# Performance work log

Measured on AMD Instinct MI355X. Metric: run time of the kernel, lower is better.

The kernel has to match this reference:

```python
import jax, jax.numpy as jnp
import numpy as np

N_NODES = 100000
N_EDGES = 1600000
D_IN = 128
D_H = 128
D_OUT = 64


def _glorot(key, shape):
    fan_in, fan_out = shape[0], shape[1]
    lim = np.sqrt(6.0 / (fan_in + fan_out)).astype(np.float32)
    return jax.random.uniform(key, shape, jnp.float32, -lim, lim)


def setup_inputs() -> dict:
    key = jax.random.key(0)
    ks = jax.random.split(key, 12)
    x = jax.random.normal(ks[0], (N_NODES, D_IN), jnp.float32)
    edge_index = jax.random.randint(ks[1], (2, N_EDGES), 0, N_NODES, jnp.int64)
    return {
        'x': x,
        'edge_index': edge_index,
        'Wl0': _glorot(ks[2], (D_IN, D_H)),  'bl0': jnp.zeros((D_H,), jnp.float32), 'Wr0': _glorot(ks[3], (D_IN, D_H)),
        'Wl1': _glorot(ks[4], (D_H, D_H)),   'bl1': jnp.zeros((D_H,), jnp.float32), 'Wr1': _glorot(ks[5], (D_H, D_H)),
        'Wl2': _glorot(ks[6], (D_H, D_H)),   'bl2': jnp.zeros((D_H,), jnp.float32), 'Wr2': _glorot(ks[7], (D_H, D_H)),
        'W':   _glorot(ks[8], (D_H, D_OUT)), 'b':   jnp.zeros((D_OUT,), jnp.float32),
    }


def _sage_conv(x, src, dst, inv_deg, Wl, bl, Wr):
    # mean aggregation of neighbor features at dst, then lin_l(agg) + lin_r(x)
    agg = jax.ops.segment_sum(x[src], dst, num_segments=N_NODES)  # [N, d]
    mean = agg * inv_deg  # [N, d]
    return mean @ Wl + bl + x @ Wr


def reference(x, edge_index, Wl0, bl0, Wr0, Wl1, bl1, Wr1, Wl2, bl2, Wr2, W, b):
    src, dst = edge_index[0], edge_index[1]
    deg = jax.ops.segment_sum(jnp.ones((N_EDGES,), jnp.float32), dst, num_segments=N_NODES)
    inv_deg = (1.0 / jnp.maximum(deg, 1.0))[:, None]  # [N, 1]
    h = jax.nn.relu(_sage_conv(x, src, dst, inv_deg, Wl0, bl0, Wr0))
    h = jax.nn.relu(_sage_conv(h, src, dst, inv_deg, Wl1, bl1, Wr1))
    h = jax.nn.relu(_sage_conv(h, src, dst, inv_deg, Wl2, bl2, Wr2))
    return h @ W + b
```

## Files before the change

### kernel.cpp

```cpp
#include <hip/hip_runtime.h>
#include <cstddef>

#define N_NODES 100000
#define N_EDGES 1600000
#define D 128
#define NB 782
#define CAP 3072
#define NBLK 1000
#define CHUNK 1600
#define WTOT (6 * 16384 + 8192)

typedef unsigned int u32;
typedef unsigned long long u64;
typedef float f32x4 __attribute__((ext_vector_type(4)));
typedef _Float16 f16x8 __attribute__((ext_vector_type(8)));

__device__ inline f16x8 mk16(u64 a, u64 b) {
  union { u64 q[2]; f16x8 v; } u;
  u.q[0] = a; u.q[1] = b;
  return u.v;
}

__device__ inline void acc8(float* a, uint2 d, float c) {
  a[0] += (float)(d.x & 0xFFu) * c;
  a[1] += (float)((d.x >> 8) & 0xFFu) * c;
  a[2] += (float)((d.x >> 16) & 0xFFu) * c;
  a[3] += (float)(d.x >> 24) * c;
  a[4] += (float)(d.y & 0xFFu) * c;
  a[5] += (float)((d.y >> 8) & 0xFFu) * c;
  a[6] += (float)((d.y >> 16) & 0xFFu) * c;
  a[7] += (float)(d.y >> 24) * c;
}


__global__ __launch_bounds__(256) void k_prep(
    const float* __restrict__ x, unsigned short* __restrict__ x16,
    unsigned char* __restrict__ x8, float* __restrict__ sx,
    const float* __restrict__ w0, const float* __restrict__ w1, const float* __restrict__ w2,
    const float* __restrict__ w3, const float* __restrict__ w4, const float* __restrict__ w5,
    const float* __restrict__ w6, unsigned short* __restrict__ wt16,
    int* __restrict__ bucket_cur) {
  int bid = blockIdx.x;
  int tid = threadIdx.x;
  if (bid < 6250) {
    int row = bid * 16 + (tid >> 4);
    int sub = tid & 15;
    const float* xr = x + (size_t)row * D + sub * 8;
    float4 v0 = *(const float4*)xr;
    float4 v1 = *(const float4*)(xr + 4);
    float vs[8] = {v0.x, v0.y, v0.z, v0.w, v1.x, v1.y, v1.z, v1.w};
    f16x8 h;
#pragma unroll
    for (int j = 0; j < 8; j++) h[j] = (_Float16)vs[j];
    *(uint4*)(x16 + (size_t)row * D + sub * 8) = __builtin_bit_cast(uint4, h);
    float m = 0.f;
#pragma unroll
    for (int j = 0; j < 8; j++) m = fmaxf(m, fabsf(vs[j]));
#pragma unroll
    for (int off = 1; off < 16; off <<= 1) m = fmaxf(m, __shfl_xor(m, off));
    m = fmaxf(m, 1e-8f);
    float inv = 127.0f / m;
    u64 pk = 0;
#pragma unroll
    for (int j = 0; j < 8; j++) {
      int qi = (int)rintf(vs[j] * inv) + 128;
      pk |= (u64)(u32)(qi & 255) << (8 * j);
    }
    *(u64*)(x8 + (size_t)row * D + sub * 8) = pk;
    if (sub == 0) sx[row] = m / 127.0f;
    return;
  }
  int i = (bid - 6250) * 256 + tid;
  if (i < NB) bucket_cur[i] = i * CAP;
  if (i >= WTOT) return;
  float v;
  if (i < 6 * 16384) {
    int m = i >> 14;
    int j = i & 16383;
    int c = j >> 7, k = j & 127;
    const float* w = (m == 0) ? w0 : (m == 1) ? w1 : (m == 2) ? w2
                   : (m == 3) ? w3 : (m == 4) ? w4 : w5;
    v = w[k * 128 + c];
  } else {
    int j = i - 6 * 16384;
    int c = j >> 7, k = j & 127;
    v = w6[k * 64 + c];
  }
  _Float16 h = (_Float16)v;
  wt16[i] = __builtin_bit_cast(unsigned short, h);
}


__global__ __launch_bounds__(256) void k_scatter(const int* __restrict__ src,
                                                 const int* __restrict__ dst,
                                                 int* __restrict__ bucket_cur,
                                                 u32* __restrict__ binned) {
  __shared__ int cnt[NB];
  __shared__ int base[NB];
  for (int i = threadIdx.x; i < NB; i += 256) cnt[i] = 0;
  __syncthreads();
  int e0 = blockIdx.x * CHUNK;
  for (int e = e0 + threadIdx.x; e < e0 + CHUNK; e += 256)
    atomicAdd(&cnt[dst[e] >> 7], 1);
  __syncthreads();
  for (int i = threadIdx.x; i < NB; i += 256) {
    int c = cnt[i];
    base[i] = c ? atomicAdd(&bucket_cur[i], c) : 0;
  }
  __syncthreads();
  for (int i = threadIdx.x; i < NB; i += 256) cnt[i] = 0;
  __syncthreads();
  for (int e = e0 + threadIdx.x; e < e0 + CHUNK; e += 256) {
    int d = dst[e];
    int b = d >> 7;
    int pos = base[b] + atomicAdd(&cnt[b], 1);
    binned[pos] = ((u32)(d & 127) << 17) | (u32)src[e];
  }
}

__global__ __launch_bounds__(256) void k_build(const u32* __restrict__ binned,
                                               const int* __restrict__ bucket_cur,
                                               int* __restrict__ row_start,
                                               int* __restrict__ row_end,
                                               float* __restrict__ inv_deg,
                                               int* __restrict__ csr_src) {
  __shared__ int deg[128], sc[128], cur[128];
  int b = blockIdx.x;
  int tid = threadIdx.x;
  int nbase = b << 7;
  int e0 = b * CAP, e1 = bucket_cur[b];
  if (tid < 128) deg[tid] = 0;
  __syncthreads();
  for (int e = e0 + tid; e < e1; e += 256)
    atomicAdd(&deg[binned[e] >> 17], 1);
  __syncthreads();
  int dv = (tid < 128) ? deg[tid] : 0;
  if (tid < 128) sc[tid] = dv;
  __syncthreads();
  for (int off = 1; off < 128; off <<= 1) {
    int t = (tid >= off && tid < 128) ? sc[tid - off] : 0;
    __syncthreads();
    if (tid < 128) sc[tid] += t;
    __syncthreads();
  }
  if (tid < 128) {
    int excl = sc[tid] - dv;
    cur[tid] = excl;
    int node = nbase + tid;
    if (node < N_NODES) {
      row_start[node] = e0 + excl;
      row_end[node] = e0 + excl + dv;
      inv_deg[node] = 1.0f / fmaxf((float)dv, 1.0f);
    }
  }
  __syncthreads();
  for (int e = e0 + tid; e < e1; e += 256) {
    u32 w = binned[e];
    int dl = w >> 17;
    int pos = e0 + atomicAdd(&cur[dl], 1);
    csr_src[pos] = (int)(w & 0x1FFFFu);
  }
}


template <bool BIASED>
__global__ __launch_bounds__(256) void k_agg(const unsigned char* __restrict__ q8,
                                             const float* __restrict__ qs,
                                             const int* __restrict__ row_start,
                                             const int* __restrict__ row_end,
                                             const float* __restrict__ inv_deg,
                                             const int* __restrict__ csr_src,
                                             unsigned short* __restrict__ out16) {
  int node = blockIdx.x * 16 + (threadIdx.x >> 4);
  if (node >= N_NODES) return;
  int sub = threadIdx.x & 15;
  int p0 = row_start[node], p1 = row_end[node];
  float a[8];
#pragma unroll
  for (int j = 0; j < 8; j++) a[j] = 0.f;
  float ssum = 0.f;
  int p = p0;
  for (; p + 8 <= p1; p += 8) {
    int s0 = csr_src[p], s1 = csr_src[p + 1], s2 = csr_src[p + 2], s3 = csr_src[p + 3];
    int s4 = csr_src[p + 4], s5 = csr_src[p + 5], s6 = csr_src[p + 6], s7 = csr_src[p + 7];
    uint2 d0 = *(const uint2*)(q8 + (size_t)s0 * D + sub * 8);
    uint2 d1 = *(const uint2*)(q8 + (size_t)s1 * D + sub * 8);
    uint2 d2 = *(const uint2*)(q8 + (size_t)s2 * D + sub * 8);
    uint2 d3 = *(const uint2*)(q8 + (size_t)s3 * D + sub * 8);
    uint2 d4 = *(const uint2*)(q8 + (size_t)s4 * D + sub * 8);
    uint2 d5 = *(const uint2*)(q8 + (size_t)s5 * D + sub * 8);
    uint2 d6 = *(const uint2*)(q8 + (size_t)s6 * D + sub * 8);
    uint2 d7 = *(const uint2*)(q8 + (size_t)s7 * D + sub * 8);
    float c0 = qs[s0], c1 = qs[s1], c2 = qs[s2], c3 = qs[s3];
    float c4 = qs[s4], c5 = qs[s5], c6 = qs[s6], c7 = qs[s7];
    acc8(a, d0, c0); acc8(a, d1, c1); acc8(a, d2, c2); acc8(a, d3, c3);
    acc8(a, d4, c4); acc8(a, d5, c5); acc8(a, d6, c6); acc8(a, d7, c7);
    if (BIASED) ssum += ((c0 + c1) + (c2 + c3)) + ((c4 + c5) + (c6 + c7));
  }
  for (; p + 2 <= p1; p += 2) {
    int s0 = csr_src[p], s1 = csr_src[p + 1];
    uint2 d0 = *(const uint2*)(q8 + (size_t)s0 * D + sub * 8);
    uint2 d1 = *(const uint2*)(q8 + (size_t)s1 * D + sub * 8);
    float c0 = qs[s0], c1 = qs[s1];
    acc8(a, d0, c0); acc8(a, d1, c1);
    if (BIASED) ssum += c0 + c1;
  }
  if (p < p1) {
    int s0 = csr_src[p];
    uint2 d0 = *(const uint2*)(q8 + (size_t)s0 * D + sub * 8);
    float c0 = qs[s0];
    acc8(a, d0, c0);
    if (BIASED) ssum += c0;
  }
  float scl = inv_deg[node];
  f16x8 o;
#pragma unroll
  for (int j = 0; j < 8; j++) {
    float v = a[j];
    if (BIASED) v -= 128.0f * ssum;
    o[j] = (_Float16)(v * scl);
  }
  *(uint4*)(out16 + (size_t)node * D + sub * 8) = __builtin_bit_cast(uint4, o);
}


__global__ __launch_bounds__(256) void k_gemm(
    const unsigned short* __restrict__ in0, const unsigned short* __restrict__ in1,
    const unsigned short* __restrict__ wt, const float* __restrict__ bias,
    unsigned short* __restrict__ outp,
    unsigned char* __restrict__ h8out, float* __restrict__ shout) {
  __shared__ u64 sI[128][9];
  __shared__ u64 sW[128][9];
  __shared__ u32 rmaxb[128];
  __shared__ unsigned char h8t[128 * 144];

  const int tid = threadIdx.x;
  const int row0 = blockIdx.x * 128;
  const int lane = tid & 63;
  const int w = tid >> 6;
  const int wr = w >> 1, wc = w & 1;
  const int lrow = lane & 15, kb = lane >> 4;
  const int sr = tid >> 2, sq = tid & 3;

  f32x4 acc[4][4];
#pragma unroll
  for (int i = 0; i < 4; i++)
#pragma unroll
    for (int j = 0; j < 4; j++) acc[i][j] = (f32x4){0.f, 0.f, 0.f, 0.f};

  u64 rA[2][2], rW[2][2];

  auto loadA = [&](int ch) {
    const unsigned short* inP = (ch >= 4) ? in1 : in0;
    const int kc = (ch & 3) * 32;
#pragma unroll
    for (int it = 0; it < 2; ++it) {
      int g = row0 + sr + it * 64;
      u64 a = 0, b = 0;
      if (g < N_NODES) {
        const u64* pp = (const u64*)(inP + (size_t)g * D + kc + sq * 8);
        a = pp[0]; b = pp[1];
      }
      rA[it][0] = a; rA[it][1] = b;
    }
  };
  auto loadW = [&](int ch) {
    const int s = ch >> 2;
    const int kc = (ch & 3) * 32;
    const unsigned short* wP = wt + (size_t)s * 16384;
#pragma unroll
    for (int it = 0; it < 2; ++it) {
      int c = sr + it * 64;
      const u64* pp = (const u64*)(wP + (size_t)c * D + kc + sq * 8);
      rW[it][0] = pp[0]; rW[it][1] = pp[1];
    }
  };

  loadA(0); loadW(0);
#pragma unroll
  for (int ch = 0; ch < 8; ++ch) {
    __syncthreads();
#pragma unroll
    for (int it = 0; it < 2; ++it) {
      int r = sr + it * 64;
      sI[r][sq * 2] = rA[it][0]; sI[r][sq * 2 + 1] = rA[it][1];
      sW[r][sq * 2] = rW[it][0]; sW[r][sq * 2 + 1] = rW[it][1];
    }
    __syncthreads();
    if (ch < 7) { loadA(ch + 1); loadW(ch + 1); }

    f16x8 fA[4], fB[4];
#pragma unroll
    for (int rt = 0; rt < 4; ++rt) {
      int rr = wr * 64 + rt * 16 + lrow;
      fA[rt] = mk16(sI[rr][kb * 2], sI[rr][kb * 2 + 1]);
    }
#pragma unroll
    for (int ct = 0; ct < 4; ++ct) {
      int cc = wc * 64 + ct * 16 + lrow;
      fB[ct] = mk16(sW[cc][kb * 2], sW[cc][kb * 2 + 1]);
    }
#pragma unroll
    for (int ct = 0; ct < 4; ++ct)
#pragma unroll
      for (int rt = 0; rt < 4; ++rt)
        acc[rt][ct] = __builtin_amdgcn_mfma_f32_16x16x32_f16(fA[rt], fB[ct], acc[rt][ct], 0, 0, 0);
  }

  if (tid < 128) rmaxb[tid] = 0;
  float bv[4];
#pragma unroll
  for (int ct = 0; ct < 4; ++ct) bv[ct] = bias[wc * 64 + ct * 16 + lrow];
#pragma unroll
  for (int ct = 0; ct < 4; ++ct)
#pragma unroll
    for (int rt = 0; rt < 4; ++rt)
#pragma unroll
      for (int r = 0; r < 4; ++r)
        acc[rt][ct][r] = fmaxf(acc[rt][ct][r] + bv[ct], 0.f);

#pragma unroll
  for (int ct = 0; ct < 4; ++ct) {
    int col = wc * 64 + ct * 16 + lrow;
#pragma unroll
    for (int rt = 0; rt < 4; ++rt) {
#pragma unroll
      for (int r = 0; r < 4; ++r) {
        int g = row0 + wr * 64 + rt * 16 + kb * 4 + r;
        if (g < N_NODES) {
          _Float16 hv = (_Float16)acc[rt][ct][r];
          outp[(size_t)g * D + col] = __builtin_bit_cast(unsigned short, hv);
        }
      }
    }
  }
  __syncthreads();
#pragma unroll
  for (int rt = 0; rt < 4; ++rt) {
#pragma unroll
    for (int r = 0; r < 4; ++r) {
      float m = fmaxf(fmaxf(acc[rt][0][r], acc[rt][1][r]),
                      fmaxf(acc[rt][2][r], acc[rt][3][r]));
      m = fmaxf(m, __shfl_xor(m, 1));
      m = fmaxf(m, __shfl_xor(m, 2));
      m = fmaxf(m, __shfl_xor(m, 4));
      m = fmaxf(m, __shfl_xor(m, 8));
      if (lrow == 0)
        atomicMax(&rmaxb[wr * 64 + rt * 16 + kb * 4 + r], __float_as_uint(m));
    }
  }
  __syncthreads();
#pragma unroll
  for (int rt = 0; rt < 4; ++rt) {
#pragma unroll
    for (int r = 0; r < 4; ++r) {
      int row = wr * 64 + rt * 16 + kb * 4 + r;
      float rm = fmaxf(__uint_as_float(rmaxb[row]), 1e-8f);
      float inv = 255.0f / rm;
#pragma unroll
      for (int ct = 0; ct < 4; ++ct) {
        u32 q = (u32)(acc[rt][ct][r] * inv + 0.5f);
        h8t[row * 144 + wc * 64 + ct * 16 + lrow] = (unsigned char)q;
      }
    }
  }
  __syncthreads();
  for (int idx = tid; idx < 128 * 8; idx += 256) {
    int row = idx >> 3, qq = idx & 7;
    int g = row0 + row;
    if (g < N_NODES)
      *(uint4*)(h8out + (size_t)g * D + qq * 16) =
          *(const uint4*)(h8t + row * 144 + qq * 16);
  }
  if (tid < 128 && row0 + tid < N_NODES)
    shout[row0 + tid] = fmaxf(__uint_as_float(rmaxb[tid]), 1e-8f) / 255.0f;
}


__global__ __launch_bounds__(256) void k_gemm2(
    const unsigned short* __restrict__ in0, const unsigned short* __restrict__ in1,
    const unsigned short* __restrict__ wt, const float* __restrict__ bias,
    const unsigned short* __restrict__ w2, const float* __restrict__ b2,
    float* __restrict__ outp) {
  __shared__ __align__(16) char smem[128 * 33 * 8 + 2 * 128 * 9 * 8];
  u64 (*sH3)[33] = (u64(*)[33])smem;
  u64 (*sI)[9] = (u64(*)[9])(smem + 128 * 33 * 8);
  u64 (*sW)[9] = (u64(*)[9])(smem + 128 * 33 * 8 + 128 * 9 * 8);
  u64 (*sW2)[33] = (u64(*)[33])(smem + 128 * 33 * 8);

  const int tid = threadIdx.x;
  const int row0 = blockIdx.x * 128;
  const int lane = tid & 63;
  const int w = tid >> 6;
  const int wr = w >> 1, wc = w & 1;
  const int lrow = lane & 15, kb = lane >> 4;
  const int sr = tid >> 2, sq = tid & 3;

  f32x4 acc[4][4];
#pragma unroll
  for (int i = 0; i < 4; i++)
#pragma unroll
    for (int j = 0; j < 4; j++) acc[i][j] = (f32x4){0.f, 0.f, 0.f, 0.f};

  u64 rA[2][2], rW[2][2];

  auto loadA = [&](int ch) {
    const unsigned short* inP = (ch >= 4) ? in1 : in0;
    const int kc = (ch & 3) * 32;
#pragma unroll
    for (int it = 0; it < 2; ++it) {
      int g = row0 + sr + it * 64;
      u64 a = 0, b = 0;
      if (g < N_NODES) {
        const u64* pp = (const u64*)(inP + (size_t)g * D + kc + sq * 8);
        a = pp[0]; b = pp[1];
      }
      rA[it][0] = a; rA[it][1] = b;
    }
  };
  auto loadW = [&](int ch) {
    const int s = ch >> 2;
    const int kc = (ch & 3) * 32;
    const unsigned short* wP = wt + (size_t)s * 16384;
#pragma unroll
    for (int it = 0; it < 2; ++it) {
      int c = sr + it * 64;
      const u64* pp = (const u64*)(wP + (size_t)c * D + kc + sq * 8);
      rW[it][0] = pp[0]; rW[it][1] = pp[1];
    }
  };

  loadA(0); loadW(0);
#pragma unroll
  for (int ch = 0; ch < 8; ++ch) {
    __syncthreads();
#pragma unroll
    for (int it = 0; it < 2; ++it) {
      int r = sr + it * 64;
      sI[r][sq * 2] = rA[it][0]; sI[r][sq * 2 + 1] = rA[it][1];
      sW[r][sq * 2] = rW[it][0]; sW[r][sq * 2 + 1] = rW[it][1];
    }
    __syncthreads();
    if (ch < 7) { loadA(ch + 1); loadW(ch + 1); }

    f16x8 fA[4], fB[4];
#pragma unroll
    for (int rt = 0; rt < 4; ++rt) {
      int rr = wr * 64 + rt * 16 + lrow;
      fA[rt] = mk16(sI[rr][kb * 2], sI[rr][kb * 2 + 1]);
    }
#pragma unroll
    for (int ct = 0; ct < 4; ++ct) {
      int cc = wc * 64 + ct * 16 + lrow;
      fB[ct] = mk16(sW[cc][kb * 2], sW[cc][kb * 2 + 1]);
    }
#pragma unroll
    for (int ct = 0; ct < 4; ++ct)
#pragma unroll
      for (int rt = 0; rt < 4; ++rt)
        acc[rt][ct] = __builtin_amdgcn_mfma_f32_16x16x32_f16(fA[rt], fB[ct], acc[rt][ct], 0, 0, 0);
  }

#pragma unroll
  for (int ct = 0; ct < 4; ++ct) {
    int col = wc * 64 + ct * 16 + lrow;
    float bv = bias[col];
#pragma unroll
    for (int rt = 0; rt < 4; ++rt) {
      int rbase = wr * 64 + rt * 16 + kb * 4;
#pragma unroll
      for (int r = 0; r < 4; ++r) {
        float v = fmaxf(acc[rt][ct][r] + bv, 0.f);
        _Float16 hv = (_Float16)v;
        ((unsigned short*)(&sH3[rbase + r][0]))[col] = __builtin_bit_cast(unsigned short, hv);
      }
    }
  }
  __syncthreads();
  for (int idx = tid; idx < 64 * 32; idx += 256) {
    int c = idx >> 5, j = idx & 31;
    sW2[c][j] = ((const u64*)(w2 + (size_t)c * D))[j];
  }
  __syncthreads();

  f32x4 acc2[4][2];
#pragma unroll
  for (int i = 0; i < 4; i++)
#pragma unroll
    for (int j = 0; j < 2; j++) acc2[i][j] = (f32x4){0.f, 0.f, 0.f, 0.f};

#pragma unroll
  for (int kc2 = 0; kc2 < 4; ++kc2) {
    f16x8 fA[4], fB[2];
#pragma unroll
    for (int rt = 0; rt < 4; ++rt) {
      int rr = wr * 64 + rt * 16 + lrow;
      fA[rt] = mk16(sH3[rr][kc2 * 8 + kb * 2], sH3[rr][kc2 * 8 + kb * 2 + 1]);
    }
#pragma unroll
    for (int ct = 0; ct < 2; ++ct) {
      int cc = wc * 32 + ct * 16 + lrow;
      fB[ct] = mk16(sW2[cc][kc2 * 8 + kb * 2], sW2[cc][kc2 * 8 + kb * 2 + 1]);
    }
#pragma unroll
    for (int ct = 0; ct < 2; ++ct)
#pragma unroll
      for (int rt = 0; rt < 4; ++rt)
        acc2[rt][ct] =
            __builtin_amdgcn_mfma_f32_16x16x32_f16(fA[rt], fB[ct], acc2[rt][ct], 0, 0, 0);
  }

#pragma unroll
  for (int ct = 0; ct < 2; ++ct) {
    int col = wc * 32 + ct * 16 + lrow;
    float bv = b2[col];
#pragma unroll
    for (int rt = 0; rt < 4; ++rt) {
#pragma unroll
      for (int r = 0; r < 4; ++r) {
        int g = row0 + wr * 64 + rt * 16 + kb * 4 + r;
        if (g < N_NODES) outp[(size_t)g * 64 + col] = acc2[rt][ct][r] + bv;
      }
    }
  }
}


extern "C" void kernel_launch(void* const* d_in, const int* in_sizes, int n_in,
                              void* d_out, int out_size, void* d_ws, size_t ws_size,
                              hipStream_t stream) {
  const float* x = (const float*)d_in[0];
  const int* edge = (const int*)d_in[1];
  const int* src = edge;
  const int* dst = edge + N_EDGES;
  const float* Wl0 = (const float*)d_in[2];
  const float* bl0 = (const float*)d_in[3];
  const float* Wr0 = (const float*)d_in[4];
  const float* Wl1 = (const float*)d_in[5];
  const float* bl1 = (const float*)d_in[6];
  const float* Wr1 = (const float*)d_in[7];
  const float* Wl2 = (const float*)d_in[8];
  const float* bl2 = (const float*)d_in[9];
  const float* Wr2 = (const float*)d_in[10];
  const float* W = (const float*)d_in[11];
  const float* b = (const float*)d_in[12];
  float* out = (float*)d_out;
  (void)ws_size; (void)n_in; (void)in_sizes; (void)out_size;

  char* ws = (char*)d_ws;
  int* bucket_cur = (int*)(ws);
  float* sx = (float*)(ws + (16ll << 10));
  float* sh = (float*)(ws + (448ll << 10));
  int* row_start = (int*)(ws + (1ll << 20));
  int* row_end = (int*)(ws + (2ll << 20));
  float* inv_deg = (float*)(ws + (3ll << 20));
  int* csr_src = (int*)(ws + (4ll << 20));
  unsigned short* wt16 = (unsigned short*)(ws + (14ll << 20));
  unsigned short* x16 = (unsigned short*)(ws + (15ll << 20));
  unsigned short* agg16 = (unsigned short*)(ws + (41ll << 20));
  unsigned short* hA = (unsigned short*)(ws + (67ll << 20));
  unsigned char* x8 = (unsigned char*)(ws + (93ll << 20));
  unsigned char* h8 = (unsigned char*)(ws + (106ll << 20));
  u32* binned = (u32*)(ws + (106ll << 20));

  k_prep<<<6250 + (WTOT + 255) / 256, 256, 0, stream>>>(
      x, x16, x8, sx, Wl0, Wr0, Wl1, Wr1, Wl2, Wr2, W, wt16, bucket_cur);
  k_scatter<<<NBLK, 256, 0, stream>>>(src, dst, bucket_cur, binned);
  k_build<<<NB, 256, 0, stream>>>(binned, bucket_cur, row_start, row_end, inv_deg, csr_src);

  const int agg_grid = (N_NODES + 15) / 16;
  const int gemm_grid = (N_NODES + 127) / 128;

  k_agg<true><<<agg_grid, 256, 0, stream>>>(x8, sx, row_start, row_end, inv_deg, csr_src, agg16);
  k_gemm<<<gemm_grid, 256, 0, stream>>>(agg16, x16, wt16 + 0, bl0, hA, h8, sh);
  k_agg<false><<<agg_grid, 256, 0, stream>>>(h8, sh, row_start, row_end, inv_deg, csr_src, agg16);
  k_gemm<<<gemm_grid, 256, 0, stream>>>(agg16, hA, wt16 + 32768, bl1, hA, h8, sh);
  k_agg<false><<<agg_grid, 256, 0, stream>>>(h8, sh, row_start, row_end, inv_deg, csr_src, agg16);
  k_gemm2<<<gemm_grid, 256, 0, stream>>>(agg16, hA, wt16 + 65536, bl2,
                                         wt16 + 98304, b, out);
}
```

Before: 286.2 us.

## Stage binned edges in LDS and write buckets out contiguously

The edge-binning scatter kernel now processes larger chunks per block. It computes per-bucket local offsets with a block-wide prefix scan and stages the packed edges in shared memory first. Each wavefront then copies whole buckets to global memory in contiguous runs, replacing scattered per-edge global stores and cutting the number of global atomics on bucket counters. The trade-off is fewer blocks (128) than the GPU has compute units, plus about 60KB of LDS per block, which lowers parallelism in this stage.

```diff
diff --git a/kernel.cpp b/kernel.cpp
--- a/kernel.cpp
+++ b/kernel.cpp
@@ -6,8 +6,8 @@
 #define D 128
 #define NB 782
 #define CAP 3072
-#define NBLK 1000
-#define CHUNK 1600
+#define NBLK 128
+#define CHUNK 12500
 #define WTOT (6 * 16384 + 8192)
 
 typedef unsigned int u32;
@@ -95,26 +95,55 @@
                                                  const int* __restrict__ dst,
                                                  int* __restrict__ bucket_cur,
                                                  u32* __restrict__ binned) {
-  __shared__ int cnt[NB];
-  __shared__ int base[NB];
-  for (int i = threadIdx.x; i < NB; i += 256) cnt[i] = 0;
-  __syncthreads();
-  int e0 = blockIdx.x * CHUNK;
-  for (int e = e0 + threadIdx.x; e < e0 + CHUNK; e += 256)
+  __shared__ int cnt[NB], lbase[NB], gbase[NB];
+  __shared__ int wsum[256];
+  __shared__ u32 stage[CHUNK];
+  const int tid = threadIdx.x;
+  for (int i = tid; i < NB; i += 256) cnt[i] = 0;
+  __syncthreads();
+  const int e0 = blockIdx.x * CHUNK;
+  for (int e = e0 + tid; e < e0 + CHUNK; e += 256)
     atomicAdd(&cnt[dst[e] >> 7], 1);
   __syncthreads();
-  for (int i = threadIdx.x; i < NB; i += 256) {
-    int c = cnt[i];
-    base[i] = c ? atomicAdd(&bucket_cur[i], c) : 0;
-  }
-  __syncthreads();
-  for (int i = threadIdx.x; i < NB; i += 256) cnt[i] = 0;
-  __syncthreads();
-  for (int e = e0 + threadIdx.x; e < e0 + CHUNK; e += 256) {
+  int c[4], s = 0;
+#pragma unroll
+  for (int j = 0; j < 4; j++) {
+    int i = tid * 4 + j;
+    c[j] = (i < NB) ? cnt[i] : 0;
+    s += c[j];
+  }
+  wsum[tid] = s;
+  __syncthreads();
+  for (int off = 1; off < 256; off <<= 1) {
+    int t = (tid >= off) ? wsum[tid - off] : 0;
+    __syncthreads();
+    wsum[tid] += t;
+    __syncthreads();
+  }
+  int run = wsum[tid] - s;
+#pragma unroll
+  for (int j = 0; j < 4; j++) {
+    int i = tid * 4 + j;
+    if (i < NB) {
+      lbase[i] = run;
+      gbase[i] = c[j] ? atomicAdd(&bucket_cur[i], c[j]) : 0;
+      run += c[j];
+    }
+  }
+  __syncthreads();
+  for (int i = tid; i < NB; i += 256) cnt[i] = 0;
+  __syncthreads();
+  for (int e = e0 + tid; e < e0 + CHUNK; e += 256) {
     int d = dst[e];
-    int b = d >> 7;
-    int pos = base[b] + atomicAdd(&cnt[b], 1);
-    binned[pos] = ((u32)(d & 127) << 17) | (u32)src[e];
+    int bkt = d >> 7;
+    int l = atomicAdd(&cnt[bkt], 1);
+    stage[lbase[bkt] + l] = ((u32)(d & 127) << 17) | (u32)src[e];
+  }
+  __syncthreads();
+  const int wv = tid >> 6, lane = tid & 63;
+  for (int bkt = wv; bkt < NB; bkt += 4) {
+    int n = cnt[bkt], lb = lbase[bkt], gb = gbase[bkt];
+    for (int k = lane; k < n; k += 64) binned[gb + k] = stage[lb + k];
   }
 }
 
@@ -549,7 +578,7 @@
 
   char* ws = (char*)d_ws;
   int* bucket_cur = (int*)(ws);
-  float* sx = (float*)(ws + (16ll << 10));
+  float* sx = (float*)(ws + (32ll << 10));
   float* sh = (float*)(ws + (448ll << 10));
   int* row_start = (int*)(ws + (1ll << 20));
   int* row_end = (int*)(ws + (2ll << 20));
```

Result: slower. 318.8 us (+11.4%).
